# Performance work log

Measured on AMD Instinct MI355X. Metric: run time of the kernel, lower is better.

## Reference

```python
import jax, jax.numpy as jnp
import numpy as np

B, C, H, W = 8, 256, 128, 128
NH, WS = 8, 8
HD = C // NH
WNH, WNW = H // WS, W // WS


def _rel_pos_index():
    coords = np.stack(np.meshgrid(np.arange(WS), np.arange(WS), indexing='ij'))  # [2,ws,ws]
    flat = coords.reshape(2, -1)
    rel = (flat[:, :, None] - flat[:, None, :]).transpose(1, 2, 0)  # [ws^2,ws^2,2]
    rel[..., 0] += WS - 1
    rel[..., 1] += WS - 1
    rel[..., 0] *= 2 * WS - 1
    return jnp.asarray(rel.sum(-1))  # [ws^2,ws^2]


def grid_sample(img, grid):
    # Bilinear, padding_mode='zeros', align_corners=True. img [N,C,H,W], grid [N,Hg,Wg,2] (x,y in [-1,1])
    N, Ci, Hi, Wi = img.shape
    gx = (grid[..., 0] + 1.0) * 0.5 * (Wi - 1)
    gy = (grid[..., 1] + 1.0) * 0.5 * (Hi - 1)
    x0 = jnp.floor(gx)
    y0 = jnp.floor(gy)
    x0i = x0.astype(jnp.int32)
    y0i = y0.astype(jnp.int32)
    wx1 = gx - x0
    wx0 = 1.0 - wx1
    wy1 = gy - y0
    wy0 = 1.0 - wy1
    nb = jnp.arange(N)[:, None, None]

    def corner(yi, xi, wgt):
        valid = (yi >= 0) & (yi < Hi) & (xi >= 0) & (xi < Wi)
        yc = jnp.clip(yi, 0, Hi - 1)
        xc = jnp.clip(xi, 0, Wi - 1)
        val = img[nb, :, yc, xc]  # [N,Hg,Wg,C]
        return val * (wgt * valid)[..., None]

    out = (corner(y0i, x0i, wy0 * wx0) + corner(y0i, x0i + 1, wy0 * wx1)
           + corner(y0i + 1, x0i, wy1 * wx0) + corner(y0i + 1, x0i + 1, wy1 * wx1))
    return jnp.transpose(out, (0, 3, 1, 2))


def setup_inputs() -> dict:
    key = jax.random.key(0)
    ks = jax.random.split(key, 10)
    f = lambda k, s, sc=1.0: jax.random.normal(k, s, dtype=jnp.float32) * sc
    return {
        'x': f(ks[0], (B, C, H, W)),
        'qkv_w': f(ks[1], (3 * C, C), 0.02),
        'qkv_b': f(ks[2], (3 * C,), 0.02),
        'bias_w': f(ks[3], (2 * NH, C), 0.02),
        'bias_b': f(ks[4], (2 * NH,), 0.02),
        'scale_w': f(ks[5], (2 * NH, C), 0.02),
        'scale_b': f(ks[6], (2 * NH,), 0.02),
        'proj_w': f(ks[7], (C, C), 0.02),
        'proj_b': f(ks[8], (C,), 0.02),
        'rpb_table': f(ks[9], ((2 * WS - 1) ** 2, NH), 0.02),
    }


def reference(x, qkv_w, qkv_b, bias_w, bias_b, scale_w, scale_b, proj_w, proj_b, rpb_table):
    scale = HD ** -0.5
    N = B * NH
    # ---- deterministic base sampling coordinates (shift=0, no padding since H,W % WS == 0) ----
    lin_w = jnp.linspace(-1.0, 1.0, W)
    lin_h = jnp.linspace(-1.0, 1.0, H)
    winref_w = lin_w.reshape(WNW, WS).mean(-1)  # window centers along width
    winref_h = lin_h.reshape(WNH, WS).mean(-1)
    off_w = jnp.arange(WS) * 2.0 / (W - 1)
    off_w = off_w - off_w.mean()
    off_h = jnp.arange(WS) * 2.0 / (H - 1)
    off_h = off_h - off_h.mean()
    base_x = jnp.broadcast_to(winref_w[None, None, :, None] + off_w[None, None, None, :], (WNH, WS, WNW, WS))
    base_y = jnp.broadcast_to((winref_h[:, None] + off_h[None, :])[:, :, None, None], (WNH, WS, WNW, WS))
    # ---- predicted per-head per-window biases & scales ----
    xp = jax.nn.leaky_relu(x.reshape(B, C, WNH, WS, WNW, WS).mean((3, 5)))  # [B,C,WNH,WNW]
    biases = (jnp.einsum('oc,bchw->bohw', bias_w, xp) + bias_b[None, :, None, None]).reshape(N, 2, WNH, WNW)
    bx = biases[:, 0] / WNW  # sampling_biases[:,0] / (w // ws)
    by = biases[:, 1] / WNH
    scales = (jnp.einsum('oc,bchw->bohw', scale_w, xp) + scale_b[None, :, None, None]).reshape(N, 2, WNH, WNW)
    sx, sy = scales[:, 0], scales[:, 1]
    # final = base + local_offsets * scale + bias (broadcast [N,WNH,1,WNW,1] over window interior)
    cx = base_x[None] + off_w[None, None, None, None, :] * sx[:, :, None, :, None] + bx[:, :, None, :, None]
    cy = base_y[None] + off_h[None, None, :, None, None] * sy[:, :, None, :, None] + by[:, :, None, :, None]
    grid = jnp.stack([cx, cy], -1).reshape(N, H, W, 2)
    # ---- qkv via 1x1 conv ----
    qkv = (jnp.einsum('oc,bchw->bohw', qkv_w, x) + qkv_b[None, :, None, None]).reshape(B, 3, NH, HD, H, W)
    q = qkv[:, 0].reshape(N, HD, H, W)
    k = qkv[:, 1].reshape(N, HD, H, W)
    v = qkv[:, 2].reshape(N, HD, H, W)
    ksamp = grid_sample(k, grid)
    vsamp = grid_sample(v, grid)

    def win(t):  # [N,HD,H,W] -> [B, nWin, NH, WS*WS, HD]
        t = t.reshape(B, NH, HD, WNH, WS, WNW, WS)
        return jnp.transpose(t, (0, 3, 5, 1, 4, 6, 2)).reshape(B, WNH * WNW, NH, WS * WS, HD)

    qw, kw, vw = win(q), win(ksamp), win(vsamp)
    rpb = jnp.transpose(rpb_table[_rel_pos_index().reshape(-1)].reshape(WS * WS, WS * WS, NH), (2, 0, 1))
    attn = jnp.einsum('bwhqd,bwhkd->bwhqk', qw, kw) * scale + rpb[None, None]
    attn = jax.nn.softmax(attn, axis=-1)
    out = jnp.einsum('bwhqk,bwhkd->bwhqd', attn, vw)
    out = out.reshape(B, WNH, WNW, NH, WS, WS, HD)
    out = jnp.transpose(out, (0, 3, 6, 1, 4, 2, 5)).reshape(B, C, H, W)
    out = jnp.einsum('oc,bchw->bohw', proj_w, out) + proj_b[None, :, None, None]
    return out
```

## Files before the change

kernel.cpp:

```cpp
#include <hip/hip_runtime.h>
#include <hip/hip_fp16.h>

#define B_ 8
#define C_ 256
#define H_ 128
#define W_ 128
#define NH_ 8
#define WS_ 8
#define HD_ 32
#define WN_ 16
#define NWIN_ 256
#define HW_ 16384

typedef unsigned short ushort_t;
typedef unsigned int uint_t;
typedef __attribute__((ext_vector_type(8))) short short8;
typedef _Float16 __attribute__((ext_vector_type(8))) half8;
typedef __attribute__((ext_vector_type(4))) float f32x4;

__device__ __forceinline__ ushort_t bf16_rtn(float x) {
    uint_t u = __float_as_uint(x);
    return (ushort_t)((u + 0x7FFFu + ((u >> 16) & 1u)) >> 16);
}
__device__ __forceinline__ uint_t bfpack(float a, float b) {
    return (uint_t)bf16_rtn(a) | ((uint_t)bf16_rtn(b) << 16);
}
__device__ __forceinline__ uint_t h2pack(float a, float b) {
    __half2 h = __floats2half2_rn(a, b);
    return __builtin_bit_cast(uint_t, h);
}

__global__ __launch_bounds__(256) void wconv_h_kernel(const float* __restrict__ w,
                            ushort_t* __restrict__ wh, int n4) {
    int i = blockIdx.x*256 + threadIdx.x;
    if (i >= n4) return;
    float4 v = ((const float4*)w)[i];
    ((uint2*)wh)[i] = make_uint2(h2pack(v.x, v.y), h2pack(v.z, v.w));
}

__global__ __launch_bounds__(256) void wconv_kernel(const float* __restrict__ w,
                            ushort_t* __restrict__ wh, int n4) {
    int i = blockIdx.x*256 + threadIdx.x;
    if (i >= n4) return;
    float4 v = ((const float4*)w)[i];
    ((uint2*)wh)[i] = make_uint2(bfpack(v.x, v.y), bfpack(v.z, v.w));
}

__global__ __launch_bounds__(256) void rpb_expand_kernel(const float* __restrict__ rpb_table,
                            float* __restrict__ rpbT) {
    int nh = blockIdx.x;
    int t = threadIdx.x;
    #pragma unroll
    for (int rr = 0; rr < 16; ++rr) {
        int e = t*16 + rr;
        int kcol = e >> 6, qrow = e & 63;
        int yq = qrow >> 3, xq = qrow & 7, yk = kcol >> 3, xk = kcol & 7;
        int idx = (yq - yk + 7)*15 + (xq - xk + 7);
        rpbT[((size_t)nh*64 + kcol)*64 + qrow] = rpb_table[idx*8 + nh];
    }
}

__global__ __launch_bounds__(256) void pool2_kernel(const float* __restrict__ xpart, float* __restrict__ xp) {
    int bc = blockIdx.x;
    int t = threadIdx.x;
    int wy = t >> 4, wxg = t & 15;
    const float* src = xpart + (size_t)bc*2048;
    float s = 0.f;
    #pragma unroll
    for (int i = 0; i < 8; ++i) s += src[(wy*8+i)*16 + wxg];
    s *= (1.f/64.f);
    xp[(size_t)bc*256 + t] = s > 0.f ? s : 0.01f*s;
}

__global__ __launch_bounds__(256) void params_kernel(const float* __restrict__ xp,
                              const float* __restrict__ bias_w, const float* __restrict__ bias_b,
                              const float* __restrict__ scale_w, const float* __restrict__ scale_b,
                              float* __restrict__ params) {
    __shared__ float xs[256];
    int blk = blockIdx.x;
    int b = blk >> 8, win = blk & 255;
    int t = threadIdx.x;
    xs[t] = xp[((size_t)(b*256 + t))*256 + win];
    __syncthreads();
    if (t < 32) {
        int which = t >> 4;
        int o = t & 15;
        const float* Wm = which ? scale_w : bias_w;
        float acc = which ? scale_b[o] : bias_b[o];
        for (int c = 0; c < 256; ++c) acc += Wm[o*256 + c] * xs[c];
        int nh = o >> 1, comp = o & 1;
        int n = b*8 + nh;
        float v = which ? acc : 3.96875f * acc;
        params[((size_t)(n*256 + win))*4 + which*2 + comp] = v;
    }
}

__global__ __launch_bounds__(256) void mgemm_qkvx_kernel(const ushort_t* __restrict__ wq,
                            const float* __restrict__ x,
                            const float* __restrict__ bias,
                            ushort_t* __restrict__ qt, ushort_t* __restrict__ kv,
                            float* __restrict__ xpart) {
    __shared__ __align__(16) uint4 Albuf[1024];
    __shared__ __align__(16) float Btile[64*129];
    uint4* B16 = (uint4*)Btile;

    int zb = blockIdx.z;
    const float* xb = x + (size_t)zb*C_*HW_;
    ushort_t* qtb = qt + (size_t)zb*HW_*256;
    ushort_t* kvb = kv + (size_t)zb*8*HW_*64;
    int o0 = blockIdx.x * 128, p0 = blockIdx.y * 128;
    int hrow = blockIdx.y;
    int t = threadIdx.x;
    int lane = t & 63, wid = t >> 6;
    int wm = wid >> 1, wn = wid & 1;
    int q = lane >> 4, rl = lane & 15;

    f32x4 acc[4][4];
    #pragma unroll
    for (int f = 0; f < 4; ++f)
        #pragma unroll
        for (int g = 0; g < 4; ++g)
            acc[f][g] = (f32x4){0.f, 0.f, 0.f, 0.f};

    int srow = t >> 1, shalf = t & 1;
    int sw = srow & 7;

    for (int ks = 0; ks < 4; ++ks) {
        int c0 = ks * 64;
        __syncthreads();
        {
            const uint4* a_h = (const uint4*)(wq + (size_t)(o0+srow)*256 + c0);
            #pragma unroll
            for (int jj = 0; jj < 4; ++jj) {
                int u = shalf*4 + jj;
                Albuf[srow*8 + (u ^ sw)] = a_h[u];
            }
        }
        {
            #pragma unroll
            for (int r = 0; r < 8; ++r) {
                int task = t + r*256;
                int cl = task >> 5, p4 = (task & 31) * 4;
                float4 v = *(const float4*)(xb + (size_t)(c0+cl)*HW_ + p0 + p4);
                float* dst = &Btile[cl*129 + p4];
                dst[0] = v.x; dst[1] = v.y; dst[2] = v.z; dst[3] = v.w;
            }
        }
        __syncthreads();
        if (blockIdx.x == 0) {
            #pragma unroll
            for (int r = 0; r < 4; ++r) {
                int task = t + r*256;
                int cl = task >> 4, wxg = task & 15;
                float s = 0.f;
                #pragma unroll
                for (int j = 0; j < 8; ++j) s += Btile[cl*129 + wxg*8 + j];
                xpart[(((size_t)zb*256 + c0+cl)*128 + hrow)*16 + wxg] = s;
            }
        }
        uint4 cvt[4];
        #pragma unroll
        for (int r = 0; r < 4; ++r) {
            int task = t + r*256;
            int pl = task >> 3, cb = (task & 7) * 8;
            float f[8];
            #pragma unroll
            for (int e = 0; e < 8; ++e) f[e] = Btile[(cb+e)*129 + pl];
            cvt[r].x = h2pack(f[0], f[1]); cvt[r].y = h2pack(f[2], f[3]);
            cvt[r].z = h2pack(f[4], f[5]); cvt[r].w = h2pack(f[6], f[7]);
        }
        __syncthreads();
        #pragma unroll
        for (int r = 0; r < 4; ++r) {
            int task = t + r*256;
            int pl = task >> 3, u = task & 7;
            B16[pl*8 + (u ^ (pl & 7))] = cvt[r];
        }
        __syncthreads();
        #pragma unroll
        for (int kk = 0; kk < 2; ++kk) {
            half8 afh[4], bfh[4];
            #pragma unroll
            for (int f = 0; f < 4; ++f) {
                int row = wm*64 + f*16 + rl;
                int u = (kk*4 + q) ^ (row & 7);
                afh[f] = __builtin_bit_cast(half8, Albuf[row*8 + u]);
            }
            #pragma unroll
            for (int g = 0; g < 4; ++g) {
                int row = wn*64 + g*16 + rl;
                int u = (kk*4 + q) ^ (row & 7);
                bfh[g] = __builtin_bit_cast(half8, B16[row*8 + u]);
            }
            #pragma unroll
            for (int f = 0; f < 4; ++f)
                #pragma unroll
                for (int g = 0; g < 4; ++g)
                    acc[f][g] = __builtin_amdgcn_mfma_f32_16x16x32_f16(afh[f], bfh[g], acc[f][g], 0, 0, 0);
        }
    }
    float* tb = Btile;
    int pl = t >> 1, half = t & 1;
    #pragma unroll
    for (int pass = 0; pass < 2; ++pass) {
        __syncthreads();
        if (wm == pass) {
            #pragma unroll
            for (int f = 0; f < 4; ++f)
                #pragma unroll
                for (int g = 0; g < 4; ++g)
                    #pragma unroll
                    for (int r = 0; r < 4; ++r)
                        tb[(f*16 + q*4 + r)*129 + wn*64 + g*16 + rl] = acc[f][g][r];
        }
        __syncthreads();
        {
            int obase = o0 + pass*64 + half*32;
            int type = obase >> 8;
            int oo = obase & 255;
            int head = oo >> 5;
            size_t pix = p0 + pl;
            ushort_t* dst = (type == 0)
                ? qtb + pix*256 + oo
                : kvb + ((size_t)head*HW_ + pix)*64 + ((type == 2) ? 32 : 0) + (oo & 31);
            #pragma unroll
            for (int u = 0; u < 4; ++u) {
                float v[8];
                #pragma unroll
                for (int e = 0; e < 8; ++e) v[e] = tb[(half*32 + u*8 + e)*129 + pl];
                float4 b0 = *(const float4*)&bias[obase + u*8];
                float4 b1 = *(const float4*)&bias[obase + u*8 + 4];
                uint4 Hv;
                Hv.x = h2pack(v[0]+b0.x, v[1]+b0.y);
                Hv.y = h2pack(v[2]+b0.z, v[3]+b0.w);
                Hv.z = h2pack(v[4]+b1.x, v[5]+b1.y);
                Hv.w = h2pack(v[6]+b1.z, v[7]+b1.w);
                *(uint4*)(dst + u*8) = Hv;
            }
        }
    }
}

__global__ __launch_bounds__(256) void mgemm_proj_kernel(const ushort_t* __restrict__ wp,
                            const ushort_t* __restrict__ at,
                            const float* __restrict__ bias, float* __restrict__ out) {
    __shared__ __align__(16) uint4 smem[2048];
    uint4* Ah = smem; uint4* Bh = smem + 1024;
    int zb = blockIdx.z;
    const ushort_t* xh = at + (size_t)zb*HW_*256;
    float* outb = out + (size_t)zb*C_*HW_;
    int o0 = blockIdx.x * 128, p0 = blockIdx.y * 128;
    int t = threadIdx.x;
    int lane = t & 63, wid = t >> 6;
    int wm = wid >> 1, wn = wid & 1;
    int q = lane >> 4, rl = lane & 15;

    f32x4 acc[4][4];
    #pragma unroll
    for (int f = 0; f < 4; ++f)
        #pragma unroll
        for (int g = 0; g < 4; ++g)
            acc[f][g] = (f32x4){0.f, 0.f, 0.f, 0.f};

    int srow = t >> 1, shalf = t & 1;
    int sw = srow & 7;

    for (int ks = 0; ks < 4; ++ks) {
        int c0 = ks * 64;
        __syncthreads();
        {
            const uint4* a_h = (const uint4*)(wp + (size_t)(o0+srow)*256 + c0);
            const uint4* b_h = (const uint4*)(xh + (size_t)(p0+srow)*256 + c0);
            #pragma unroll
            for (int jj = 0; jj < 4; ++jj) {
                int u = shalf*4 + jj;
                int d = srow*8 + (u ^ sw);
                Ah[d] = a_h[u]; Bh[d] = b_h[u];
            }
        }
        __syncthreads();
        #pragma unroll
        for (int kk = 0; kk < 2; ++kk) {
            short8 afh[4], bfh[4];
            #pragma unroll
            for (int f = 0; f < 4; ++f) {
                int row = wm*64 + f*16 + rl;
                int u = (kk*4 + q) ^ (row & 7);
                afh[f] = __builtin_bit_cast(short8, Ah[row*8 + u]);
            }
            #pragma unroll
            for (int g = 0; g < 4; ++g) {
                int row = wn*64 + g*16 + rl;
                int u = (kk*4 + q) ^ (row & 7);
                bfh[g] = __builtin_bit_cast(short8, Bh[row*8 + u]);
            }
            #pragma unroll
            for (int f = 0; f < 4; ++f)
                #pragma unroll
                for (int g = 0; g < 4; ++g)
                    acc[f][g] = __builtin_amdgcn_mfma_f32_16x16x32_bf16(afh[f], bfh[g], acc[f][g], 0, 0, 0);
        }
    }
    #pragma unroll
    for (int f = 0; f < 4; ++f) {
        float4 bb = *(const float4*)&bias[o0 + wm*64 + f*16 + q*4];
        float bbv[4] = {bb.x, bb.y, bb.z, bb.w};
        #pragma unroll
        for (int g = 0; g < 4; ++g) {
            int p = p0 + wn*64 + g*16 + rl;
            #pragma unroll
            for (int r = 0; r < 4; ++r) {
                int o = o0 + wm*64 + f*16 + q*4 + r;
                outb[(size_t)o*HW_ + p] = acc[f][g][r] + bbv[r];
            }
        }
    }
}

__global__ __launch_bounds__(256) void attn_kernel(const ushort_t* __restrict__ qt,
                            const ushort_t* __restrict__ kv,
                            const float* __restrict__ params_,
                            const float* __restrict__ rpbT,
                            ushort_t* __restrict__ at) {
    __shared__ __align__(16) ushort_t smem[64*40 + 64*40 + 32*72 + 64*40];
    ushort_t (*Q_lds)[40]   = (ushort_t(*)[40])smem;
    ushort_t (*K_lds)[40]   = (ushort_t(*)[40])(smem + 2560);
    ushort_t (*VT_lds)[72]  = (ushort_t(*)[72])(smem + 5120);
    ushort_t (*P_lds)[72]   = (ushort_t(*)[72])smem;
    ushort_t (*OUT_lds)[40] = (ushort_t(*)[40])(smem + 5120 + 2304);

    int b = blockIdx.y;
    int blk = blockIdx.x;
    int win = blk >> 3, nh = blk & 7;
    int wy = win >> 4, wx = win & 15;
    int t = threadIdx.x;
    int lane = t & 63, wid = t >> 6;

    const float* pp = params_ + ((size_t)((b*8 + nh)*256 + win))*4;
    float ox = pp[0], oy = pp[1], sx = pp[2], sy = pp[3];

    const ushort_t* qtb = qt + (size_t)b*HW_*256;
    const ushort_t* kvb = kv + ((size_t)(b*8 + nh))*HW_*64;
    ushort_t* ath = at + (size_t)b*HW_*256;

    {
        int tok = t >> 2, cg = t & 3;
        int i = tok >> 3, j = tok & 7;
        size_t pix = (size_t)(wy*8 + i)*W_ + wx*8 + j;
        *(uint4*)&Q_lds[tok][cg*8] = *(const uint4*)(qtb + pix*256 + nh*32 + cg*8);
    }
    {
        int tokq = lane >> 3, sub = lane & 7;
        #pragma unroll
        for (int r = 0; r < 2; ++r) {
            int tok = wid*16 + r*8 + tokq;
            int i = tok >> 3, j = tok & 7;
            int h = wy*8 + i, wpx = wx*8 + j;
            float gx = (float)wpx + ((float)j - 3.5f)*sx + ox;
            float gy = (float)h  + ((float)i - 3.5f)*sy + oy;
            float x0f = floorf(gx), y0f = floorf(gy);
            int x0 = (int)x0f, y0 = (int)y0f;
            float wx1 = gx - x0f, wy1 = gy - y0f;
            float wxz = 1.f - wx1, wyz = 1.f - wy1;
            int x1 = x0 + 1, y1 = y0 + 1;
            float m00 = wyz*wxz * ((y0>=0 && y0<H_ && x0>=0 && x0<W_) ? 1.f : 0.f);
            float m01 = wyz*wx1 * ((y0>=0 && y0<H_ && x1>=0 && x1<W_) ? 1.f : 0.f);
            float m10 = wy1*wxz * ((y1>=0 && y1<H_ && x0>=0 && x0<W_) ? 1.f : 0.f);
            float m11 = wy1*wx1 * ((y1>=0 && y1<H_ && x1>=0 && x1<W_) ? 1.f : 0.f);
            int x0c = min(max(x0,0),W_-1), x1c = min(max(x1,0),W_-1);
            int y0c = min(max(y0,0),H_-1), y1c = min(max(y1,0),H_-1);
            size_t p00 = (size_t)y0c*W_ + x0c, p01 = (size_t)y0c*W_ + x1c;
            size_t p10 = (size_t)y1c*W_ + x0c, p11 = (size_t)y1c*W_ + x1c;
            __half2 a0 = __float2half2_rn(0.f), a1 = a0, a2 = a0, a3 = a0;
            #define CORNER(PIX, M) { \
                uint4 u = *(const uint4*)(kvb + (PIX)*64 + sub*8); \
                __half2 wv = __float2half2_rn(M); \
                a0 = __hfma2(__builtin_bit_cast(__half2, u.x), wv, a0); \
                a1 = __hfma2(__builtin_bit_cast(__half2, u.y), wv, a1); \
                a2 = __hfma2(__builtin_bit_cast(__half2, u.z), wv, a2); \
                a3 = __hfma2(__builtin_bit_cast(__half2, u.w), wv, a3); }
            CORNER(p00, m00)
            CORNER(p01, m01)
            CORNER(p10, m10)
            CORNER(p11, m11)
            #undef CORNER
            if (sub < 4) {
                uint4 Kv;
                Kv.x = __builtin_bit_cast(uint_t, a0); Kv.y = __builtin_bit_cast(uint_t, a1);
                Kv.z = __builtin_bit_cast(uint_t, a2); Kv.w = __builtin_bit_cast(uint_t, a3);
                *(uint4*)&K_lds[tok][sub*8] = Kv;
            } else {
                int d0 = (sub - 4)*8;
                VT_lds[d0+0][tok] = __half_as_ushort(__low2half(a0));
                VT_lds[d0+1][tok] = __half_as_ushort(__high2half(a0));
                VT_lds[d0+2][tok] = __half_as_ushort(__low2half(a1));
                VT_lds[d0+3][tok] = __half_as_ushort(__high2half(a1));
                VT_lds[d0+4][tok] = __half_as_ushort(__low2half(a2));
                VT_lds[d0+5][tok] = __half_as_ushort(__high2half(a2));
                VT_lds[d0+6][tok] = __half_as_ushort(__low2half(a3));
                VT_lds[d0+7][tok] = __half_as_ushort(__high2half(a3));
            }
        }
    }
    __syncthreads();

    int q = lane >> 4, rl = lane & 15;
    const float scale = 0.17677669529663687f;

    half8 a_frag = *(const half8*)&Q_lds[wid*16 + rl][q*8];
    half8 b_frag[4];
    #pragma unroll
    for (int g = 0; g < 4; ++g)
        b_frag[g] = *(const half8*)&K_lds[g*16 + rl][q*8];
    __syncthreads();

    f32x4 accS[4];
    #pragma unroll
    for (int g = 0; g < 4; ++g)
        accS[g] = __builtin_amdgcn_mfma_f32_16x16x32_f16(a_frag, b_frag[g], (f32x4){0.f,0.f,0.f,0.f}, 0, 0, 0);

    float Sv[4][4];
    const float* rpbb = rpbT + (size_t)nh*4096;
    int m0 = wid*16 + q*4;
    #pragma unroll
    for (int g = 0; g < 4; ++g) {
        float4 rv = *(const float4*)&rpbb[(g*16 + rl)*64 + m0];
        Sv[g][0] = accS[g][0]*scale + rv.x;
        Sv[g][1] = accS[g][1]*scale + rv.y;
        Sv[g][2] = accS[g][2]*scale + rv.z;
        Sv[g][3] = accS[g][3]*scale + rv.w;
    }
    float inv[4];
    #pragma unroll
    for (int r = 0; r < 4; ++r) {
        float pm = fmaxf(fmaxf(Sv[0][r], Sv[1][r]), fmaxf(Sv[2][r], Sv[3][r]));
        pm = fmaxf(pm, __shfl_xor(pm, 1));
        pm = fmaxf(pm, __shfl_xor(pm, 2));
        pm = fmaxf(pm, __shfl_xor(pm, 4));
        pm = fmaxf(pm, __shfl_xor(pm, 8));
        float s = 0.f;
        #pragma unroll
        for (int g = 0; g < 4; ++g) {
            float e = __expf(Sv[g][r] - pm);
            Sv[g][r] = e;
            s += e;
        }
        s += __shfl_xor(s, 1);
        s += __shfl_xor(s, 2);
        s += __shfl_xor(s, 4);
        s += __shfl_xor(s, 8);
        inv[r] = 1.f / s;
    }
    #pragma unroll
    for (int r = 0; r < 4; ++r) {
        int m = wid*16 + q*4 + r;
        #pragma unroll
        for (int g = 0; g < 4; ++g)
            P_lds[m][g*16 + rl] = __half_as_ushort(__float2half(Sv[g][r]*inv[r]));
    }

    f32x4 accO[2] = {(f32x4){0.f,0.f,0.f,0.f}, (f32x4){0.f,0.f,0.f,0.f}};
    #pragma unroll
    for (int ks = 0; ks < 2; ++ks) {
        half8 p_frag = *(const half8*)&P_lds[wid*16 + rl][ks*32 + q*8];
        #pragma unroll
        for (int g2 = 0; g2 < 2; ++g2) {
            half8 v_frag = *(const half8*)&VT_lds[g2*16 + rl][ks*32 + q*8];
            accO[g2] = __builtin_amdgcn_mfma_f32_16x16x32_f16(p_frag, v_frag, accO[g2], 0, 0, 0);
        }
    }
    #pragma unroll
    for (int r = 0; r < 4; ++r) {
        int m = wid*16 + q*4 + r;
        OUT_lds[m][rl]      = bf16_rtn(accO[0][r]);
        OUT_lds[m][16 + rl] = bf16_rtn(accO[1][r]);
    }
    __syncthreads();
    {
        int tok = t >> 2, cg = t & 3;
        int i2 = tok >> 3, j2 = tok & 7;
        size_t pix = (size_t)(wy*8 + i2)*W_ + wx*8 + j2;
        *(uint4*)(ath + pix*256 + nh*32 + cg*8) = *(const uint4*)&OUT_lds[tok][cg*8];
    }
}

extern "C" void kernel_launch(void* const* d_in, const int* in_sizes, int n_in,
                              void* d_out, int out_size, void* d_ws, size_t ws_size,
                              hipStream_t stream) {
    const float* x       = (const float*)d_in[0];
    const float* qkv_w   = (const float*)d_in[1];
    const float* qkv_b   = (const float*)d_in[2];
    const float* bias_w  = (const float*)d_in[3];
    const float* bias_b  = (const float*)d_in[4];
    const float* scale_w = (const float*)d_in[5];
    const float* scale_b = (const float*)d_in[6];
    const float* proj_w  = (const float*)d_in[7];
    const float* proj_b  = (const float*)d_in[8];
    const float* rpb     = (const float*)d_in[9];
    float* out = (float*)d_out;

    char* ws = (char*)d_ws;
    float*    xp       = (float*)ws;     ws += (size_t)524288*4;
    float*    params   = (float*)ws;     ws += (size_t)65536*4;
    float*    xpart    = (float*)ws;     ws += (size_t)4194304*4;
    float*    rpbT     = (float*)ws;     ws += (size_t)8*4096*4;
    ushort_t* wq       = (ushort_t*)ws;  ws += (size_t)768*256*2;
    ushort_t* wp       = (ushort_t*)ws;  ws += (size_t)256*256*2;
    ushort_t* at       = (ushort_t*)ws;  ws += (size_t)B_*HW_*256*2;
    ushort_t* qt       = (ushort_t*)ws;  ws += (size_t)B_*HW_*256*2;
    ushort_t* kv       = (ushort_t*)ws;

    wconv_h_kernel<<<dim3(192), 256, 0, stream>>>(qkv_w, wq, 768*256/4);
    wconv_kernel  <<<dim3(64),  256, 0, stream>>>(proj_w, wp, 256*256/4);
    rpb_expand_kernel<<<dim3(NH_), 256, 0, stream>>>(rpb, rpbT);
    mgemm_qkvx_kernel<<<dim3(6, 128, B_), 256, 0, stream>>>(wq, x, qkv_b, qt, kv, xpart);
    pool2_kernel <<<dim3(B_*C_), 256, 0, stream>>>(xpart, xp);
    params_kernel<<<dim3(B_*NWIN_), 256, 0, stream>>>(xp, bias_w, bias_b, scale_w, scale_b, params);
    attn_kernel<<<dim3(NH_*NWIN_, B_), 256, 0, stream>>>(qt, kv, params, rpbT, at);
    mgemm_proj_kernel<<<dim3(2, 128, B_), 256, 0, stream>>>(wp, at, proj_b, out);
}
```

Baseline: 362.2 us.

## Load x tile once per block and loop over all QKV output channels

The QKV GEMM is restructured so each block loads a 128-pixel row of x for all 256 input channels once and keeps it as f16 MFMA B-fragments in registers, then iterates over all 768 output channels, reading weight fragments directly from global memory. Before, six blocks each reread and converted the same x tile. This removes redundant fp32 x reads and conversions, but cuts the grid from 6144 to 1024 blocks and raises register pressure, which may lower occupancy. A-operand reuse now comes from cache rather than shared memory.

```diff
diff --git a/kernel.cpp b/kernel.cpp
--- a/kernel.cpp
+++ b/kernel.cpp
@@ -95,147 +95,122 @@
     }
 }
 
-__global__ __launch_bounds__(256) void mgemm_qkvx_kernel(const ushort_t* __restrict__ wq,
+__global__ __launch_bounds__(256) void mgemm_qkvr_kernel(const ushort_t* __restrict__ wq,
                             const float* __restrict__ x,
                             const float* __restrict__ bias,
                             ushort_t* __restrict__ qt, ushort_t* __restrict__ kv,
                             float* __restrict__ xpart) {
-    __shared__ __align__(16) uint4 Albuf[1024];
     __shared__ __align__(16) float Btile[64*129];
-    uint4* B16 = (uint4*)Btile;
-
-    int zb = blockIdx.z;
+    int zb = blockIdx.y;
+    int hrow = blockIdx.x;
+    int p0 = hrow * 128;
     const float* xb = x + (size_t)zb*C_*HW_;
     ushort_t* qtb = qt + (size_t)zb*HW_*256;
     ushort_t* kvb = kv + (size_t)zb*8*HW_*64;
-    int o0 = blockIdx.x * 128, p0 = blockIdx.y * 128;
-    int hrow = blockIdx.y;
     int t = threadIdx.x;
     int lane = t & 63, wid = t >> 6;
-    int wm = wid >> 1, wn = wid & 1;
-    int q = lane >> 4, rl = lane & 15;
-
-    f32x4 acc[4][4];
-    #pragma unroll
-    for (int f = 0; f < 4; ++f)
-        #pragma unroll
-        for (int g = 0; g < 4; ++g)
-            acc[f][g] = (f32x4){0.f, 0.f, 0.f, 0.f};
-
-    int srow = t >> 1, shalf = t & 1;
-    int sw = srow & 7;
+    int qi = lane >> 4, rl = lane & 15;
+
+    half8 bfrag[2][8];
 
     for (int ks = 0; ks < 4; ++ks) {
-        int c0 = ks * 64;
+        int c0 = ks*64;
         __syncthreads();
-        {
-            const uint4* a_h = (const uint4*)(wq + (size_t)(o0+srow)*256 + c0);
-            #pragma unroll
-            for (int jj = 0; jj < 4; ++jj) {
-                int u = shalf*4 + jj;
-                Albuf[srow*8 + (u ^ sw)] = a_h[u];
-            }
-        }
-        {
-            #pragma unroll
-            for (int r = 0; r < 8; ++r) {
-                int task = t + r*256;
-                int cl = task >> 5, p4 = (task & 31) * 4;
-                float4 v = *(const float4*)(xb + (size_t)(c0+cl)*HW_ + p0 + p4);
-                float* dst = &Btile[cl*129 + p4];
-                dst[0] = v.x; dst[1] = v.y; dst[2] = v.z; dst[3] = v.w;
-            }
+        #pragma unroll
+        for (int r = 0; r < 8; ++r) {
+            int task = t + r*256;
+            int cl = task >> 5, p4 = (task & 31)*4;
+            float4 v = *(const float4*)(xb + (size_t)(c0+cl)*HW_ + p0 + p4);
+            float* dst = &Btile[cl*129 + p4];
+            dst[0]=v.x; dst[1]=v.y; dst[2]=v.z; dst[3]=v.w;
         }
         __syncthreads();
-        if (blockIdx.x == 0) {
-            #pragma unroll
-            for (int r = 0; r < 4; ++r) {
-                int task = t + r*256;
-                int cl = task >> 4, wxg = task & 15;
-                float s = 0.f;
-                #pragma unroll
-                for (int j = 0; j < 8; ++j) s += Btile[cl*129 + wxg*8 + j];
-                xpart[(((size_t)zb*256 + c0+cl)*128 + hrow)*16 + wxg] = s;
-            }
-        }
-        uint4 cvt[4];
         #pragma unroll
         for (int r = 0; r < 4; ++r) {
             int task = t + r*256;
-            int pl = task >> 3, cb = (task & 7) * 8;
-            float f[8];
-            #pragma unroll
-            for (int e = 0; e < 8; ++e) f[e] = Btile[(cb+e)*129 + pl];
-            cvt[r].x = h2pack(f[0], f[1]); cvt[r].y = h2pack(f[2], f[3]);
-            cvt[r].z = h2pack(f[4], f[5]); cvt[r].w = h2pack(f[6], f[7]);
-        }
-        __syncthreads();
-        #pragma unroll
-        for (int r = 0; r < 4; ++r) {
-            int task = t + r*256;
-            int pl = task >> 3, u = task & 7;
-            B16[pl*8 + (u ^ (pl & 7))] = cvt[r];
-        }
-        __syncthreads();
-        #pragma unroll
-        for (int kk = 0; kk < 2; ++kk) {
-            half8 afh[4], bfh[4];
+            int cl = task >> 4, wxg = task & 15;
+            float s = 0.f;
+            #pragma unroll
+            for (int j = 0; j < 8; ++j) s += Btile[cl*129 + wxg*8 + j];
+            xpart[(((size_t)zb*256 + c0+cl)*128 + hrow)*16 + wxg] = s;
+        }
+        #pragma unroll
+        for (int g = 0; g < 2; ++g) {
+            int pix = wid*32 + g*16 + rl;
+            #pragma unroll
+            for (int k2 = 0; k2 < 2; ++k2) {
+                float f[8];
+                #pragma unroll
+                for (int e = 0; e < 8; ++e)
+                    f[e] = Btile[(k2*32 + qi*8 + e)*129 + pix];
+                uint4 c;
+                c.x = h2pack(f[0],f[1]); c.y = h2pack(f[2],f[3]);
+                c.z = h2pack(f[4],f[5]); c.w = h2pack(f[6],f[7]);
+                bfrag[g][ks*2 + k2] = __builtin_bit_cast(half8, c);
+            }
+        }
+    }
+
+    for (int oc = 0; oc < 6; ++oc) {
+        f32x4 acc[8][2];
+        #pragma unroll
+        for (int f = 0; f < 8; ++f) {
+            acc[f][0] = (f32x4){0.f,0.f,0.f,0.f};
+            acc[f][1] = (f32x4){0.f,0.f,0.f,0.f};
+        }
+        const ushort_t* wbase = wq + (size_t)oc*128*256 + (size_t)rl*256 + qi*8;
+        #pragma unroll
+        for (int kk = 0; kk < 8; ++kk) {
+            #pragma unroll
+            for (int fh = 0; fh < 2; ++fh) {
+                half8 af[4];
+                #pragma unroll
+                for (int f4 = 0; f4 < 4; ++f4)
+                    af[f4] = *(const half8*)(wbase + (size_t)(fh*4 + f4)*16*256 + kk*32);
+                #pragma unroll
+                for (int f4 = 0; f4 < 4; ++f4) {
+                    acc[fh*4+f4][0] = __builtin_amdgcn_mfma_f32_16x16x32_f16(af[f4], bfrag[0][kk], acc[fh*4+f4][0], 0, 0, 0);
+                    acc[fh*4+f4][1] = __builtin_amdgcn_mfma_f32_16x16x32_f16(af[f4], bfrag[1][kk], acc[fh*4+f4][1], 0, 0, 0);
+                }
+            }
+        }
+        float* tb = Btile;
+        int pl = t >> 1, halfi = t & 1;
+        #pragma unroll
+        for (int pass = 0; pass < 2; ++pass) {
+            __syncthreads();
             #pragma unroll
             for (int f = 0; f < 4; ++f) {
-                int row = wm*64 + f*16 + rl;
-                int u = (kk*4 + q) ^ (row & 7);
-                afh[f] = __builtin_bit_cast(half8, Albuf[row*8 + u]);
-            }
-            #pragma unroll
-            for (int g = 0; g < 4; ++g) {
-                int row = wn*64 + g*16 + rl;
-                int u = (kk*4 + q) ^ (row & 7);
-                bfh[g] = __builtin_bit_cast(half8, B16[row*8 + u]);
-            }
-            #pragma unroll
-            for (int f = 0; f < 4; ++f)
-                #pragma unroll
-                for (int g = 0; g < 4; ++g)
-                    acc[f][g] = __builtin_amdgcn_mfma_f32_16x16x32_f16(afh[f], bfh[g], acc[f][g], 0, 0, 0);
-        }
-    }
-    float* tb = Btile;
-    int pl = t >> 1, half = t & 1;
-    #pragma unroll
-    for (int pass = 0; pass < 2; ++pass) {
-        __syncthreads();
-        if (wm == pass) {
-            #pragma unroll
-            for (int f = 0; f < 4; ++f)
-                #pragma unroll
-                for (int g = 0; g < 4; ++g)
+                #pragma unroll
+                for (int g = 0; g < 2; ++g)
                     #pragma unroll
                     for (int r = 0; r < 4; ++r)
-                        tb[(f*16 + q*4 + r)*129 + wn*64 + g*16 + rl] = acc[f][g][r];
-        }
-        __syncthreads();
-        {
-            int obase = o0 + pass*64 + half*32;
-            int type = obase >> 8;
-            int oo = obase & 255;
-            int head = oo >> 5;
-            size_t pix = p0 + pl;
-            ushort_t* dst = (type == 0)
-                ? qtb + pix*256 + oo
-                : kvb + ((size_t)head*HW_ + pix)*64 + ((type == 2) ? 32 : 0) + (oo & 31);
-            #pragma unroll
-            for (int u = 0; u < 4; ++u) {
-                float v[8];
-                #pragma unroll
-                for (int e = 0; e < 8; ++e) v[e] = tb[(half*32 + u*8 + e)*129 + pl];
-                float4 b0 = *(const float4*)&bias[obase + u*8];
-                float4 b1 = *(const float4*)&bias[obase + u*8 + 4];
-                uint4 Hv;
-                Hv.x = h2pack(v[0]+b0.x, v[1]+b0.y);
-                Hv.y = h2pack(v[2]+b0.z, v[3]+b0.w);
-                Hv.z = h2pack(v[4]+b1.x, v[5]+b1.y);
-                Hv.w = h2pack(v[6]+b1.z, v[7]+b1.w);
-                *(uint4*)(dst + u*8) = Hv;
+                        tb[(f*16 + qi*4 + r)*129 + wid*32 + g*16 + rl] = acc[pass*4+f][g][r];
+            }
+            __syncthreads();
+            {
+                int obase = oc*128 + pass*64 + halfi*32;
+                int type = obase >> 8;
+                int oo = obase & 255;
+                int head = oo >> 5;
+                size_t pix = p0 + pl;
+                ushort_t* dst = (type == 0)
+                    ? qtb + pix*256 + oo
+                    : kvb + ((size_t)head*HW_ + pix)*64 + ((type == 2) ? 32 : 0) + (oo & 31);
+                #pragma unroll
+                for (int u = 0; u < 4; ++u) {
+                    float v[8];
+                    #pragma unroll
+                    for (int e = 0; e < 8; ++e) v[e] = tb[(halfi*32 + u*8 + e)*129 + pl];
+                    float4 b0 = *(const float4*)&bias[obase + u*8];
+                    float4 b1 = *(const float4*)&bias[obase + u*8 + 4];
+                    uint4 Hv;
+                    Hv.x = h2pack(v[0]+b0.x, v[1]+b0.y);
+                    Hv.y = h2pack(v[2]+b0.z, v[3]+b0.w);
+                    Hv.z = h2pack(v[4]+b1.x, v[5]+b1.y);
+                    Hv.w = h2pack(v[6]+b1.z, v[7]+b1.w);
+                    *(uint4*)(dst + u*8) = Hv;
+                }
             }
         }
     }
@@ -513,7 +488,7 @@
     wconv_h_kernel<<<dim3(192), 256, 0, stream>>>(qkv_w, wq, 768*256/4);
     wconv_kernel  <<<dim3(64),  256, 0, stream>>>(proj_w, wp, 256*256/4);
     rpb_expand_kernel<<<dim3(NH_), 256, 0, stream>>>(rpb, rpbT);
-    mgemm_qkvx_kernel<<<dim3(6, 128, B_), 256, 0, stream>>>(wq, x, qkv_b, qt, kv, xpart);
+    mgemm_qkvr_kernel<<<dim3(128, B_), 256, 0, stream>>>(wq, x, qkv_b, qt, kv, xpart);
     pool2_kernel <<<dim3(B_*C_), 256, 0, stream>>>(xpart, xp);
     params_kernel<<<dim3(B_*NWIN_), 256, 0, stream>>>(xp, bias_w, bias_b, scale_w, scale_b, params);
     attn_kernel<<<dim3(NH_*NWIN_, B_), 256, 0, stream>>>(qt, kv, params, rpbT, at);
```

After: 421.6 us. 1.16x slower.
